# Kernel tuning notes

Hardware: AMD Instinct MI355X
Metric: run time of the kernel (lower is better)

## Reference

```python
import jax, jax.numpy as jnp
import numpy as np

B, N, DIM, H, KVAL = 16, 1024, 128, 8, 4  # b divisible by K*K=16; mask batch = B//(K*K)=1


def setup_inputs() -> dict:
    key = jax.random.key(0)
    ks = jax.random.split(key, 6)
    x = jax.random.normal(ks[0], (B, N, DIM), jnp.float32)
    mask = (jax.random.uniform(ks[1], (B // (KVAL * KVAL), N - 1)) < 0.9).astype(jnp.float32)
    maps = (jax.random.uniform(ks[2], (B, N - 1)) < 0.9).astype(jnp.float32)
    Wqkv = jax.random.normal(ks[3], (DIM, 3 * DIM), jnp.float32) / np.sqrt(DIM)
    Wout = jax.random.normal(ks[4], (DIM, DIM), jnp.float32) / np.sqrt(DIM)
    bout = jnp.zeros((DIM,), jnp.float32)
    return {"x": x, "mask": mask, "maps": maps, "Wqkv": Wqkv, "Wout": Wout,
            "bout": bout, "K": KVAL}


def reference(x, mask, maps, Wqkv, Wout, bout, K):
    b, n, dim = x.shape
    h = H
    d = dim // h
    scale = dim ** -0.5
    qkv = x @ Wqkv                                  # [b, n, 3*dim]
    q, k, v = jnp.split(qkv, 3, axis=-1)

    def to_heads(t):
        return t.reshape(b, n, h, d).transpose(0, 2, 1, 3)  # [b, h, n, d]

    q, k, v = to_heads(q), to_heads(k), to_heads(v)
    dots = jnp.einsum('bhid,bhjd->bhij', q, k) * scale      # [b, h, n, n]
    mask_value = -jnp.finfo(dots.dtype).max

    # block mask: pad first key position with 1, broadcast over K*K batch block
    kk = K * K
    m = jnp.pad(mask, ((0, 0), (1, 0)), constant_values=1.0)  # [b//kk, n]
    dots = dots.reshape(b // kk, kk, h, n, n)
    m5 = m[:, None, None, None, :]
    dots = dots * m5 + mask_value * (1.0 - m5)
    dots = dots.reshape(b, h, n, n)

    # map mask: boolean fill per batch element
    mp = jnp.pad(maps, ((0, 0), (1, 0)), constant_values=1.0)  # [b, n]
    dots = jnp.where(mp[:, None, None, :] != 0, dots, mask_value)

    attn = jax.nn.softmax(dots, axis=-1)
    out = jnp.einsum('bhij,bhjd->bhid', attn, v)            # [b, h, n, d]
    out = out.transpose(0, 2, 1, 3).reshape(b, n, dim)      # [b, n, dim]
    return out @ Wout + bout
```

## Files before the change

kernel.cpp:

```cpp
#include <hip/hip_runtime.h>
#include <math.h>

#define B_   16
#define N_   1024
#define DIM_ 128
#define H_   8
#define D_   16
#define BH_  128

typedef unsigned short u16;
typedef unsigned int   u32;
typedef __attribute__((ext_vector_type(8))) short short8;
typedef __attribute__((ext_vector_type(4))) float f32x4;

__device__ __forceinline__ float bf2f(u16 u) {
    union { u32 i; float f; } c; c.i = ((u32)u) << 16; return c.f;
}
__device__ __forceinline__ u16 f2bf(float f) {
    union { float f; u32 i; } c; c.f = f;
    u32 r = c.i + 0x7FFFu + ((c.i >> 16) & 1u);
    return (u16)(r >> 16);
}
__device__ __forceinline__ u32 pack2bf(float a, float b) {
    union { float f; u32 i; } ca, cb; ca.f = a; cb.f = b;
    return ((ca.i + 0x8000u) >> 16) | ((cb.i + 0x8000u) & 0xFFFF0000u);
}
struct bfpair { short hi, lo; };
__device__ __forceinline__ bfpair splitv(float v) {
    u16 h = f2bf(v);
    bfpair p;
    p.hi = (short)h;
    p.lo = (short)f2bf(v - bf2f(h));
    return p;
}

#define SCALE_L2E (0.08838834764831845f * 1.4426950408889634f)

__global__ __launch_bounds__(256) void qkv_kernel(
    const float* __restrict__ x, const float* __restrict__ Wqkv,
    const float* __restrict__ maskp, const float* __restrict__ mapsp,
    u16* __restrict__ qws, u16* __restrict__ kws, u16* __restrict__ vtws)
{
    const int tid  = threadIdx.x;
    const int wave = tid >> 6, lane = tid & 63;
    const int i16  = lane & 15, quad = lane >> 4;
    const int cb   = blockIdx.x % 6;
    const int rb   = blockIdx.x / 6;
    const int row_m = rb * 64 + wave * 16;

    const float* xp = x + (size_t)(row_m + i16) * 128;

    f32x4 acc0 = {0,0,0,0}, acc1 = {0,0,0,0}, acc2 = {0,0,0,0}, acc3 = {0,0,0,0};

    #pragma unroll
    for (int ks = 0; ks < 4; ks++) {
        const int k0 = ks * 32 + quad * 8;
        const float4 xa = *(const float4*)(xp + k0);
        const float4 xb = *(const float4*)(xp + k0 + 4);
        short8 a_hi, a_lo;
        {
            bfpair p;
            p = splitv(xa.x); a_hi[0] = p.hi; a_lo[0] = p.lo;
            p = splitv(xa.y); a_hi[1] = p.hi; a_lo[1] = p.lo;
            p = splitv(xa.z); a_hi[2] = p.hi; a_lo[2] = p.lo;
            p = splitv(xa.w); a_hi[3] = p.hi; a_lo[3] = p.lo;
            p = splitv(xb.x); a_hi[4] = p.hi; a_lo[4] = p.lo;
            p = splitv(xb.y); a_hi[5] = p.hi; a_lo[5] = p.lo;
            p = splitv(xb.z); a_hi[6] = p.hi; a_lo[6] = p.lo;
            p = splitv(xb.w); a_hi[7] = p.hi; a_lo[7] = p.lo;
        }

        #define CT_STEP(CT, ACC) { \
            const float* wp = Wqkv + (size_t)k0 * 384 + (cb * 64 + CT * 16 + i16); \
            short8 b_hi, b_lo; \
            bfpair q; \
            q = splitv(wp[0*384]); b_hi[0] = q.hi; b_lo[0] = q.lo; \
            q = splitv(wp[1*384]); b_hi[1] = q.hi; b_lo[1] = q.lo; \
            q = splitv(wp[2*384]); b_hi[2] = q.hi; b_lo[2] = q.lo; \
            q = splitv(wp[3*384]); b_hi[3] = q.hi; b_lo[3] = q.lo; \
            q = splitv(wp[4*384]); b_hi[4] = q.hi; b_lo[4] = q.lo; \
            q = splitv(wp[5*384]); b_hi[5] = q.hi; b_lo[5] = q.lo; \
            q = splitv(wp[6*384]); b_hi[6] = q.hi; b_lo[6] = q.lo; \
            q = splitv(wp[7*384]); b_hi[7] = q.hi; b_lo[7] = q.lo; \
            ACC = __builtin_amdgcn_mfma_f32_16x16x32_bf16(a_hi, b_hi, ACC, 0, 0, 0); \
            ACC = __builtin_amdgcn_mfma_f32_16x16x32_bf16(a_lo, b_hi, ACC, 0, 0, 0); \
            ACC = __builtin_amdgcn_mfma_f32_16x16x32_bf16(a_hi, b_lo, ACC, 0, 0, 0); \
        }
        CT_STEP(0, acc0)
        CT_STEP(1, acc1)
        CT_STEP(2, acc2)
        CT_STEP(3, acc3)
        #undef CT_STEP
    }

    const int which = (cb * 64) >> 7;
    const int row   = row_m + quad * 4;
    const int bb    = row >> 10, n = row & 1023;

    float vm[4];
    if (which == 2) {
        #pragma unroll
        for (int r = 0; r < 4; r++) {
            const int nr = n + r;
            vm[r] = (nr == 0) ? 1.0f
                  : ((maskp[nr - 1] != 0.0f && mapsp[bb * (N_ - 1) + nr - 1] != 0.0f)
                     ? 1.0f : 0.0f);
        }
    }

    #define STORE_CT(CT, ACC) { \
        const int c  = (cb * 64 + CT * 16) & 127; \
        const int h  = c >> 4; \
        const int bh = bb * 8 + h; \
        const int dd = i16; \
        if (which == 0) { \
            u16* p = qws + ((size_t)(bh * N_ + n)) * 16 + dd; \
            p[0]  = f2bf(ACC[0] * SCALE_L2E); p[16] = f2bf(ACC[1] * SCALE_L2E); \
            p[32] = f2bf(ACC[2] * SCALE_L2E); p[48] = f2bf(ACC[3] * SCALE_L2E); \
        } else if (which == 1) { \
            u16* p = kws + ((size_t)(bh * N_ + n)) * 16 + dd; \
            p[0]  = f2bf(ACC[0]); p[16] = f2bf(ACC[1]); \
            p[32] = f2bf(ACC[2]); p[48] = f2bf(ACC[3]); \
        } else { \
            *(ushort4*)(vtws + ((size_t)(bh * 16 + dd)) * N_ + n) = \
                make_ushort4(f2bf(ACC[0] * vm[0]), f2bf(ACC[1] * vm[1]), \
                             f2bf(ACC[2] * vm[2]), f2bf(ACC[3] * vm[3])); \
        } }
    STORE_CT(0, acc0)
    STORE_CT(1, acc1)
    STORE_CT(2, acc2)
    STORE_CT(3, acc3)
    #undef STORE_CT
}

__global__ __launch_bounds__(256) void attn_kernel(
    const u16* __restrict__ qws, const u16* __restrict__ kws, const u16* __restrict__ vtws,
    const float* __restrict__ maskp, const float* __restrict__ mapsp,
    u16* __restrict__ attn)
{
    __shared__ u16 mbf[N_];
    const int tid = threadIdx.x;
    const int qt  = blockIdx.x;
    const int bh  = blockIdx.y;
    const int bb  = bh >> 3, h = bh & 7;
    for (int j = tid; j < N_; j += 256) {
        bool valid = (j == 0) ? true
                   : ((maskp[j - 1] != 0.0f) && (mapsp[bb * (N_ - 1) + j - 1] != 0.0f));
        mbf[j] = valid ? (u16)0x3F80 : (u16)0;
    }
    __syncthreads();

    const int wave = tid >> 6, lane = tid & 63;
    const int i16 = lane & 15, quad = lane >> 4;
    const int qrow0 = qt * 64 + wave * 16;
    const int perm = ((i16 & 12) << 1) | (i16 & 3);

    const short8 zero8 = {0,0,0,0,0,0,0,0};
    short8 qf = zero8;
    if (lane < 32)
        qf = *(const short8*)(qws + ((size_t)(bh * N_ + qrow0 + i16)) * 16 + quad * 8);

    const u16* kpA = kws + ((size_t)(bh * N_ + perm)) * 16 + quad * 8;
    const u16* kpB = kpA + 4 * 16;
    const u16* vp  = vtws + ((size_t)(bh * 16 + i16)) * N_ + quad * 8;
    const u16* mp  = &mbf[quad * 8];

    f32x4 o    = {0.f, 0.f, 0.f, 0.f};
    f32x4 lacc = {0.f, 0.f, 0.f, 0.f};
    const f32x4 zc = {0.f, 0.f, 0.f, 0.f};

    #pragma unroll 2
    for (int j0 = 0; j0 < N_; j0 += 32) {
        short8 kfA = *(const short8*)kpA;
        short8 kfB = *(const short8*)kpB;
        kpA += 32 * 16; kpB += 32 * 16;

        f32x4 stA = __builtin_amdgcn_mfma_f32_16x16x32_bf16(kfA, qf, zc, 0, 0, 0);
        f32x4 stB = __builtin_amdgcn_mfma_f32_16x16x32_bf16(kfB, qf, zc, 0, 0, 0);
        float pA[4], pB[4];
        #pragma unroll
        for (int r = 0; r < 4; r++) {
            pA[r] = __builtin_amdgcn_exp2f(stA[r]);
            pB[r] = __builtin_amdgcn_exp2f(stB[r]);
        }
        union { short8 s; u32 w[4]; } pk;
        pk.w[0] = pack2bf(pA[0], pA[1]);
        pk.w[1] = pack2bf(pA[2], pA[3]);
        pk.w[2] = pack2bf(pB[0], pB[1]);
        pk.w[3] = pack2bf(pB[2], pB[3]);

        short8 vf = *(const short8*)vp;
        short8 mf = *(const short8*)(mp + j0);
        vp += 32;
        o    = __builtin_amdgcn_mfma_f32_16x16x32_bf16(vf, pk.s, o,    0, 0, 0);
        lacc = __builtin_amdgcn_mfma_f32_16x16x32_bf16(mf, pk.s, lacc, 0, 0, 0);
    }

    const float inv = 1.0f / lacc[0];
    ushort4 pkout = make_ushort4(f2bf(o[0] * inv), f2bf(o[1] * inv),
                                 f2bf(o[2] * inv), f2bf(o[3] * inv));
    *(ushort4*)(attn + ((size_t)(bb * N_ + qrow0 + i16)) * DIM_ + h * 16 + quad * 4) = pkout;
}

__global__ __launch_bounds__(256) void out_kernel(
    const u16* __restrict__ attnw, const float* __restrict__ Wout,
    const float* __restrict__ boutp, float* __restrict__ outp)
{
    const int tid  = threadIdx.x;
    const int wave = tid >> 6, lane = tid & 63;
    const int i16  = lane & 15, quad = lane >> 4;
    const int cb   = blockIdx.x & 1;
    const int rb   = blockIdx.x >> 1;
    const int row_m = rb * 64 + wave * 16;

    const u16* ap = attnw + (size_t)(row_m + i16) * 128;

    f32x4 acc0 = {0,0,0,0}, acc1 = {0,0,0,0}, acc2 = {0,0,0,0}, acc3 = {0,0,0,0};

    #pragma unroll
    for (int ks = 0; ks < 4; ks++) {
        const int k0 = ks * 32 + quad * 8;
        const short8 a = *(const short8*)(ap + k0);

        #define CT_STEP(CT, ACC) { \
            const float* wp = Wout + (size_t)k0 * 128 + (cb * 64 + CT * 16 + i16); \
            short8 b_hi, b_lo; \
            bfpair q; \
            q = splitv(wp[0*128]); b_hi[0] = q.hi; b_lo[0] = q.lo; \
            q = splitv(wp[1*128]); b_hi[1] = q.hi; b_lo[1] = q.lo; \
            q = splitv(wp[2*128]); b_hi[2] = q.hi; b_lo[2] = q.lo; \
            q = splitv(wp[3*128]); b_hi[3] = q.hi; b_lo[3] = q.lo; \
            q = splitv(wp[4*128]); b_hi[4] = q.hi; b_lo[4] = q.lo; \
            q = splitv(wp[5*128]); b_hi[5] = q.hi; b_lo[5] = q.lo; \
            q = splitv(wp[6*128]); b_hi[6] = q.hi; b_lo[6] = q.lo; \
            q = splitv(wp[7*128]); b_hi[7] = q.hi; b_lo[7] = q.lo; \
            ACC = __builtin_amdgcn_mfma_f32_16x16x32_bf16(a, b_hi, ACC, 0, 0, 0); \
            ACC = __builtin_amdgcn_mfma_f32_16x16x32_bf16(a, b_lo, ACC, 0, 0, 0); \
        }
        CT_STEP(0, acc0)
        CT_STEP(1, acc1)
        CT_STEP(2, acc2)
        CT_STEP(3, acc3)
        #undef CT_STEP
    }

    const int row = row_m + quad * 4;
    #define STORE_CT(CT, ACC) { \
        const int col = cb * 64 + CT * 16 + i16; \
        const float bo = boutp[col]; \
        float* op = outp + (size_t)row * 128 + col; \
        op[0 * 128] = ACC[0] + bo; \
        op[1 * 128] = ACC[1] + bo; \
        op[2 * 128] = ACC[2] + bo; \
        op[3 * 128] = ACC[3] + bo; \
    }
    STORE_CT(0, acc0)
    STORE_CT(1, acc1)
    STORE_CT(2, acc2)
    STORE_CT(3, acc3)
    #undef STORE_CT
}

extern "C" void kernel_launch(void* const* d_in, const int* in_sizes, int n_in,
                              void* d_out, int out_size, void* d_ws, size_t ws_size,
                              hipStream_t stream) {
    const float* x    = (const float*)d_in[0];
    const float* mask = (const float*)d_in[1];
    const float* maps = (const float*)d_in[2];
    const float* Wqkv = (const float*)d_in[3];
    const float* Wout = (const float*)d_in[4];
    const float* bout = (const float*)d_in[5];
    u16* qws  = (u16*)d_ws;
    u16* kws  = qws  + (size_t)BH_ * N_ * D_;
    u16* vtws = kws  + (size_t)BH_ * N_ * D_;
    u16* attn = vtws + (size_t)BH_ * N_ * D_;

    qkv_kernel<<<dim3(1536), dim3(256), 0, stream>>>(x, Wqkv, mask, maps, qws, kws, vtws);
    attn_kernel<<<dim3(16, 128), dim3(256), 0, stream>>>(qws, kws, vtws, mask, maps, attn);
    out_kernel<<<dim3(512), dim3(256), 0, stream>>>(attn, Wout, bout, (float*)d_out);
}
```

Before: 150.4 us.

## Fold key mask into padded K bias column and tile four query blocks per wave

The key-validity mask moves out of the attention kernel. K is padded to 32 columns, with an extra column holding 0 or -inf that the Q fragment multiplies by a ones entry, so the exponent itself zeroes masked keys. The LDS mask table, its barrier and the V-side masking all go away. Each wave now handles 64 query rows (four 16-row tiles), so every K/V fragment load is reused four times. The bf16 hi/lo split in the QKV GEMM becomes cheaper truncation-based bit packing. The costs are a larger K buffer, more registers, fewer blocks (512), and truncation instead of rounding in the split.

```diff
diff --git a/kernel.cpp b/kernel.cpp
--- a/kernel.cpp
+++ b/kernel.cpp
@@ -25,21 +25,29 @@
     union { float f; u32 i; } ca, cb; ca.f = a; cb.f = b;
     return ((ca.i + 0x8000u) >> 16) | ((cb.i + 0x8000u) & 0xFFFF0000u);
 }
-struct bfpair { short hi, lo; };
-__device__ __forceinline__ bfpair splitv(float v) {
-    u16 h = f2bf(v);
-    bfpair p;
-    p.hi = (short)h;
-    p.lo = (short)f2bf(v - bf2f(h));
-    return p;
-}
+__device__ __forceinline__ u32 fbits(float f) {
+    union { float f; u32 i; } c; c.f = f; return c.i;
+}
+__device__ __forceinline__ float fval(u32 i) {
+    union { u32 i; float f; } c; c.i = i; return c.f;
+}
+__device__ __forceinline__ u32 pk_hi(float a, float b) {
+    return (fbits(a) >> 16) | (fbits(b) & 0xFFFF0000u);
+}
+__device__ __forceinline__ float residf(float a) {
+    return a - fval(fbits(a) & 0xFFFF0000u);
+}
+union frag8 { short8 s; u32 w[4]; };
+
+#define BF_ONE  ((short)0x3F80)
+#define BF_NINF ((u16)0xFF80)
 
 #define SCALE_L2E (0.08838834764831845f * 1.4426950408889634f)
 
 __global__ __launch_bounds__(256) void qkv_kernel(
     const float* __restrict__ x, const float* __restrict__ Wqkv,
     const float* __restrict__ maskp, const float* __restrict__ mapsp,
-    u16* __restrict__ qws, u16* __restrict__ kws, u16* __restrict__ vtws)
+    u16* __restrict__ qws, u16* __restrict__ kws2, u16* __restrict__ vtws)
 {
     const int tid  = threadIdx.x;
     const int wave = tid >> 6, lane = tid & 63;
@@ -57,34 +65,28 @@
         const int k0 = ks * 32 + quad * 8;
         const float4 xa = *(const float4*)(xp + k0);
         const float4 xb = *(const float4*)(xp + k0 + 4);
-        short8 a_hi, a_lo;
-        {
-            bfpair p;
-            p = splitv(xa.x); a_hi[0] = p.hi; a_lo[0] = p.lo;
-            p = splitv(xa.y); a_hi[1] = p.hi; a_lo[1] = p.lo;
-            p = splitv(xa.z); a_hi[2] = p.hi; a_lo[2] = p.lo;
-            p = splitv(xa.w); a_hi[3] = p.hi; a_lo[3] = p.lo;
-            p = splitv(xb.x); a_hi[4] = p.hi; a_lo[4] = p.lo;
-            p = splitv(xb.y); a_hi[5] = p.hi; a_lo[5] = p.lo;
-            p = splitv(xb.z); a_hi[6] = p.hi; a_lo[6] = p.lo;
-            p = splitv(xb.w); a_hi[7] = p.hi; a_lo[7] = p.lo;
-        }
+        frag8 a_hi, a_lo;
+        a_hi.w[0] = pk_hi(xa.x, xa.y); a_hi.w[1] = pk_hi(xa.z, xa.w);
+        a_hi.w[2] = pk_hi(xb.x, xb.y); a_hi.w[3] = pk_hi(xb.z, xb.w);
+        a_lo.w[0] = pk_hi(residf(xa.x), residf(xa.y));
+        a_lo.w[1] = pk_hi(residf(xa.z), residf(xa.w));
+        a_lo.w[2] = pk_hi(residf(xb.x), residf(xb.y));
+        a_lo.w[3] = pk_hi(residf(xb.z), residf(xb.w));
 
         #define CT_STEP(CT, ACC) { \
             const float* wp = Wqkv + (size_t)k0 * 384 + (cb * 64 + CT * 16 + i16); \
-            short8 b_hi, b_lo; \
-            bfpair q; \
-            q = splitv(wp[0*384]); b_hi[0] = q.hi; b_lo[0] = q.lo; \
-            q = splitv(wp[1*384]); b_hi[1] = q.hi; b_lo[1] = q.lo; \
-            q = splitv(wp[2*384]); b_hi[2] = q.hi; b_lo[2] = q.lo; \
-            q = splitv(wp[3*384]); b_hi[3] = q.hi; b_lo[3] = q.lo; \
-            q = splitv(wp[4*384]); b_hi[4] = q.hi; b_lo[4] = q.lo; \
-            q = splitv(wp[5*384]); b_hi[5] = q.hi; b_lo[5] = q.lo; \
-            q = splitv(wp[6*384]); b_hi[6] = q.hi; b_lo[6] = q.lo; \
-            q = splitv(wp[7*384]); b_hi[7] = q.hi; b_lo[7] = q.lo; \
-            ACC = __builtin_amdgcn_mfma_f32_16x16x32_bf16(a_hi, b_hi, ACC, 0, 0, 0); \
-            ACC = __builtin_amdgcn_mfma_f32_16x16x32_bf16(a_lo, b_hi, ACC, 0, 0, 0); \
-            ACC = __builtin_amdgcn_mfma_f32_16x16x32_bf16(a_hi, b_lo, ACC, 0, 0, 0); \
+            const float w0 = wp[0*384], w1 = wp[1*384], w2 = wp[2*384], w3 = wp[3*384]; \
+            const float w4 = wp[4*384], w5 = wp[5*384], w6 = wp[6*384], w7 = wp[7*384]; \
+            frag8 b_hi, b_lo; \
+            b_hi.w[0] = pk_hi(w0, w1); b_hi.w[1] = pk_hi(w2, w3); \
+            b_hi.w[2] = pk_hi(w4, w5); b_hi.w[3] = pk_hi(w6, w7); \
+            b_lo.w[0] = pk_hi(residf(w0), residf(w1)); \
+            b_lo.w[1] = pk_hi(residf(w2), residf(w3)); \
+            b_lo.w[2] = pk_hi(residf(w4), residf(w5)); \
+            b_lo.w[3] = pk_hi(residf(w6), residf(w7)); \
+            ACC = __builtin_amdgcn_mfma_f32_16x16x32_bf16(a_hi.s, b_hi.s, ACC, 0, 0, 0); \
+            ACC = __builtin_amdgcn_mfma_f32_16x16x32_bf16(a_lo.s, b_hi.s, ACC, 0, 0, 0); \
+            ACC = __builtin_amdgcn_mfma_f32_16x16x32_bf16(a_hi.s, b_lo.s, ACC, 0, 0, 0); \
         }
         CT_STEP(0, acc0)
         CT_STEP(1, acc1)
@@ -96,17 +98,6 @@
     const int which = (cb * 64) >> 7;
     const int row   = row_m + quad * 4;
     const int bb    = row >> 10, n = row & 1023;
-
-    float vm[4];
-    if (which == 2) {
-        #pragma unroll
-        for (int r = 0; r < 4; r++) {
-            const int nr = n + r;
-            vm[r] = (nr == 0) ? 1.0f
-                  : ((maskp[nr - 1] != 0.0f && mapsp[bb * (N_ - 1) + nr - 1] != 0.0f)
-                     ? 1.0f : 0.0f);
-        }
-    }
 
     #define STORE_CT(CT, ACC) { \
         const int c  = (cb * 64 + CT * 16) & 127; \
@@ -118,13 +109,21 @@
             p[0]  = f2bf(ACC[0] * SCALE_L2E); p[16] = f2bf(ACC[1] * SCALE_L2E); \
             p[32] = f2bf(ACC[2] * SCALE_L2E); p[48] = f2bf(ACC[3] * SCALE_L2E); \
         } else if (which == 1) { \
-            u16* p = kws + ((size_t)(bh * N_ + n)) * 16 + dd; \
-            p[0]  = f2bf(ACC[0]); p[16] = f2bf(ACC[1]); \
-            p[32] = f2bf(ACC[2]); p[48] = f2bf(ACC[3]); \
+            u16* p = kws2 + ((size_t)(bh * N_ + n)) * 32 + dd; \
+            p[0]  = f2bf(ACC[0]); p[32] = f2bf(ACC[1]); \
+            p[64] = f2bf(ACC[2]); p[96] = f2bf(ACC[3]); \
+            if (dd == 0) { \
+                _Pragma("unroll") \
+                for (int r = 0; r < 4; r++) { \
+                    const int nr = n + r; \
+                    const bool valid = (nr == 0) || \
+                        (maskp[nr - 1] != 0.0f && mapsp[bb * (N_ - 1) + nr - 1] != 0.0f); \
+                    kws2[((size_t)(bh * N_ + nr)) * 32 + 16] = valid ? (u16)0 : BF_NINF; \
+                } \
+            } \
         } else { \
             *(ushort4*)(vtws + ((size_t)(bh * 16 + dd)) * N_ + n) = \
-                make_ushort4(f2bf(ACC[0] * vm[0]), f2bf(ACC[1] * vm[1]), \
-                             f2bf(ACC[2] * vm[2]), f2bf(ACC[3] * vm[3])); \
+                make_ushort4(f2bf(ACC[0]), f2bf(ACC[1]), f2bf(ACC[2]), f2bf(ACC[3])); \
         } }
     STORE_CT(0, acc0)
     STORE_CT(1, acc1)
@@ -134,74 +133,92 @@
 }
 
 __global__ __launch_bounds__(256) void attn_kernel(
-    const u16* __restrict__ qws, const u16* __restrict__ kws, const u16* __restrict__ vtws,
-    const float* __restrict__ maskp, const float* __restrict__ mapsp,
+    const u16* __restrict__ qws, const u16* __restrict__ kws2, const u16* __restrict__ vtws,
     u16* __restrict__ attn)
 {
-    __shared__ u16 mbf[N_];
-    const int tid = threadIdx.x;
-    const int qt  = blockIdx.x;
-    const int bh  = blockIdx.y;
-    const int bb  = bh >> 3, h = bh & 7;
-    for (int j = tid; j < N_; j += 256) {
-        bool valid = (j == 0) ? true
-                   : ((maskp[j - 1] != 0.0f) && (mapsp[bb * (N_ - 1) + j - 1] != 0.0f));
-        mbf[j] = valid ? (u16)0x3F80 : (u16)0;
-    }
-    __syncthreads();
-
+    const int tid  = threadIdx.x;
     const int wave = tid >> 6, lane = tid & 63;
-    const int i16 = lane & 15, quad = lane >> 4;
-    const int qrow0 = qt * 64 + wave * 16;
+    const int i16  = lane & 15, quad = lane >> 4;
+    const int bh   = blockIdx.x;
+    const int qb   = blockIdx.y;
+    const int bb   = bh >> 3, h = bh & 7;
+    const int qrow0 = qb * 256 + wave * 64;
     const int perm = ((i16 & 12) << 1) | (i16 & 3);
 
     const short8 zero8 = {0,0,0,0,0,0,0,0};
-    short8 qf = zero8;
-    if (lane < 32)
-        qf = *(const short8*)(qws + ((size_t)(bh * N_ + qrow0 + i16)) * 16 + quad * 8);
-
-    const u16* kpA = kws + ((size_t)(bh * N_ + perm)) * 16 + quad * 8;
-    const u16* kpB = kpA + 4 * 16;
+    const short8 ones8 = {BF_ONE,BF_ONE,BF_ONE,BF_ONE,BF_ONE,BF_ONE,BF_ONE,BF_ONE};
+
+    short8 qf0 = zero8, qf1 = zero8, qf2 = zero8, qf3 = zero8;
+    if (lane < 32) {
+        const u16* qp = qws + ((size_t)(bh * N_ + qrow0 + i16)) * 16 + quad * 8;
+        qf0 = *(const short8*)(qp);
+        qf1 = *(const short8*)(qp + 256);
+        qf2 = *(const short8*)(qp + 512);
+        qf3 = *(const short8*)(qp + 768);
+    } else if (lane < 48) {
+        qf0[0] = BF_ONE; qf1[0] = BF_ONE; qf2[0] = BF_ONE; qf3[0] = BF_ONE;
+    }
+
+    const u16* kpA = kws2 + ((size_t)(bh * N_ + perm)) * 32 + quad * 8;
+    const u16* kpB = kpA + 4 * 32;
     const u16* vp  = vtws + ((size_t)(bh * 16 + i16)) * N_ + quad * 8;
-    const u16* mp  = &mbf[quad * 8];
-
-    f32x4 o    = {0.f, 0.f, 0.f, 0.f};
-    f32x4 lacc = {0.f, 0.f, 0.f, 0.f};
+
+    f32x4 o0 = {0,0,0,0}, o1 = {0,0,0,0}, o2 = {0,0,0,0}, o3 = {0,0,0,0};
+    f32x4 l0 = {0,0,0,0}, l1 = {0,0,0,0}, l2 = {0,0,0,0}, l3 = {0,0,0,0};
     const f32x4 zc = {0.f, 0.f, 0.f, 0.f};
 
     #pragma unroll 2
     for (int j0 = 0; j0 < N_; j0 += 32) {
-        short8 kfA = *(const short8*)kpA;
-        short8 kfB = *(const short8*)kpB;
-        kpA += 32 * 16; kpB += 32 * 16;
-
-        f32x4 stA = __builtin_amdgcn_mfma_f32_16x16x32_bf16(kfA, qf, zc, 0, 0, 0);
-        f32x4 stB = __builtin_amdgcn_mfma_f32_16x16x32_bf16(kfB, qf, zc, 0, 0, 0);
-        float pA[4], pB[4];
-        #pragma unroll
-        for (int r = 0; r < 4; r++) {
-            pA[r] = __builtin_amdgcn_exp2f(stA[r]);
-            pB[r] = __builtin_amdgcn_exp2f(stB[r]);
+        const short8 kfA = *(const short8*)kpA;
+        const short8 kfB = *(const short8*)kpB;
+        const short8 vf  = *(const short8*)vp;
+        kpA += 32 * 32; kpB += 32 * 32; vp += 32;
+
+        #define TILE(QF, O, L) { \
+            f32x4 stA = __builtin_amdgcn_mfma_f32_16x16x32_bf16(kfA, QF, zc, 0, 0, 0); \
+            f32x4 stB = __builtin_amdgcn_mfma_f32_16x16x32_bf16(kfB, QF, zc, 0, 0, 0); \
+            float pA0 = __builtin_amdgcn_exp2f(stA[0]); \
+            float pA1 = __builtin_amdgcn_exp2f(stA[1]); \
+            float pA2 = __builtin_amdgcn_exp2f(stA[2]); \
+            float pA3 = __builtin_amdgcn_exp2f(stA[3]); \
+            float pB0 = __builtin_amdgcn_exp2f(stB[0]); \
+            float pB1 = __builtin_amdgcn_exp2f(stB[1]); \
+            float pB2 = __builtin_amdgcn_exp2f(stB[2]); \
+            float pB3 = __builtin_amdgcn_exp2f(stB[3]); \
+            frag8 pk; \
+            pk.w[0] = pack2bf(pA0, pA1); pk.w[1] = pack2bf(pA2, pA3); \
+            pk.w[2] = pack2bf(pB0, pB1); pk.w[3] = pack2bf(pB2, pB3); \
+            O = __builtin_amdgcn_mfma_f32_16x16x32_bf16(vf,    pk.s, O, 0, 0, 0); \
+            L = __builtin_amdgcn_mfma_f32_16x16x32_bf16(ones8, pk.s, L, 0, 0, 0); \
         }
-        union { short8 s; u32 w[4]; } pk;
-        pk.w[0] = pack2bf(pA[0], pA[1]);
-        pk.w[1] = pack2bf(pA[2], pA[3]);
-        pk.w[2] = pack2bf(pB[0], pB[1]);
-        pk.w[3] = pack2bf(pB[2], pB[3]);
-
-        short8 vf = *(const short8*)vp;
-        short8 mf = *(const short8*)(mp + j0);
-        vp += 32;
-        o    = __builtin_amdgcn_mfma_f32_16x16x32_bf16(vf, pk.s, o,    0, 0, 0);
-        lacc = __builtin_amdgcn_mfma_f32_16x16x32_bf16(mf, pk.s, lacc, 0, 0, 0);
-    }
-
-    const float inv = 1.0f / lacc[0];
-    ushort4 pkout = make_ushort4(f2bf(o[0] * inv), f2bf(o[1] * inv),
-                                 f2bf(o[2] * inv), f2bf(o[3] * inv));
-    *(ushort4*)(attn + ((size_t)(bb * N_ + qrow0 + i16)) * DIM_ + h * 16 + quad * 4) = pkout;
-}
-
+        TILE(qf0, o0, l0)
+        TILE(qf1, o1, l1)
+        TILE(qf2, o2, l2)
+        TILE(qf3, o3, l3)
+        #undef TILE
+    }
+
+    #define OUT_T(T, O, L) { \
+        const float inv = 1.0f / L[0]; \
+        ushort4 pko = make_ushort4(f2bf(O[0] * inv), f2bf(O[1] * inv), \
+                                   f2bf(O[2] * inv), f2bf(O[3] * inv)); \
+        *(ushort4*)(attn + ((size_t)(bb * N_ + qrow0 + T * 16 + i16)) * DIM_ \
+                    + h * 16 + quad * 4) = pko; }
+    OUT_T(0, o0, l0)
+    OUT_T(1, o1, l1)
+    OUT_T(2, o2, l2)
+    OUT_T(3, o3, l3)
+    #undef OUT_T
+}
+
+struct bfpair { short hi, lo; };
+__device__ __forceinline__ bfpair splitv(float v) {
+    u16 h = f2bf(v);
+    bfpair p;
+    p.hi = (short)h;
+    p.lo = (short)f2bf(v - bf2f(h));
+    return p;
+}
 __global__ __launch_bounds__(256) void out_kernel(
     const u16* __restrict__ attnw, const float* __restrict__ Wout,
     const float* __restrict__ boutp, float* __restrict__ outp)
@@ -271,11 +288,11 @@
     const float* Wout = (const float*)d_in[4];
     const float* bout = (const float*)d_in[5];
     u16* qws  = (u16*)d_ws;
-    u16* kws  = qws  + (size_t)BH_ * N_ * D_;
-    u16* vtws = kws  + (size_t)BH_ * N_ * D_;
-    u16* attn = vtws + (size_t)BH_ * N_ * D_;
-
-    qkv_kernel<<<dim3(1536), dim3(256), 0, stream>>>(x, Wqkv, mask, maps, qws, kws, vtws);
-    attn_kernel<<<dim3(16, 128), dim3(256), 0, stream>>>(qws, kws, vtws, mask, maps, attn);
+    u16* kws2 = qws  + (size_t)BH_ * N_ * 16;
+    u16* vtws = kws2 + (size_t)BH_ * N_ * 32;
+    u16* attn = vtws + (size_t)BH_ * N_ * 16;
+
+    qkv_kernel<<<dim3(1536), dim3(256), 0, stream>>>(x, Wqkv, mask, maps, qws, kws2, vtws);
+    attn_kernel<<<dim3(128, 4), dim3(256), 0, stream>>>(qws, kws2, vtws, attn);
     out_kernel<<<dim3(512), dim3(256), 0, stream>>>(attn, Wout, bout, (float*)d_out);
 }
```

Measured after the change: 130.7 us. 13.1% less time.
